# Kernel tuning notes

Measured on AMD Instinct MI355X. Metric: run time of the kernel, lower is better.

The kernel has to match this reference:

```python
import jax, jax.numpy as jnp
import numpy as np

B, K, N, M = 32, 128, 128, 256  # batch, num_classes(==n_dim), n_dim, samples-per-matrix
EPSILON = 0.1
LAMBDA_SOFTMAX = 0.1
LEARNING_RATE = 0.01
BN_EPS = 1e-5


def setup_inputs() -> dict:
    key = jax.random.key(0)
    k1, k2, k3 = jax.random.split(key, 3)
    x = jax.random.normal(k1, (B, N, M), dtype=jnp.float32)
    A = jax.random.normal(k2, (K, N, N), dtype=jnp.float32) * 0.1
    EC_proto = jnp.einsum('kij,klj->kil', A, A)  # per-class PSD prototype covariances (K,N,N)
    EC_count = jax.random.uniform(k3, (K,), dtype=jnp.float32, minval=1.0, maxval=100.0)
    return {"x": x, "EC_proto": EC_proto, "EC_count": EC_count}


def reference(x, EC_proto, EC_count):
    n = x.shape[1]
    dtype = x.dtype
    # BatchNorm1d(num_classes, affine=False, track_running_stats=False): batch stats over (N, L)
    mean = x.mean(axis=(0, 2), keepdims=True)
    var = x.var(axis=(0, 2), keepdims=True)  # biased variance, as torch uses for normalization
    x = (x - mean) / jnp.sqrt(var + BN_EPS)

    eye = jnp.eye(n, dtype=dtype)
    total = EC_count.sum()
    has_counts = total > 1e-6

    # E branch: global expansion operator
    e_alpha = jnp.where(has_counts, n / (EPSILON * EPSILON * total), jnp.zeros((), dtype))
    e = e_alpha * jnp.linalg.inv(e_alpha * EC_proto.sum(0) + eye)  # (N,N)
    e_x_z = jnp.einsum('ij,bjm->bim', e, x)  # (B,N,M)

    # C branch: per-class compression operators
    bool_depth = (EC_count != 0).astype(dtype)  # (K,)
    count_fix = EC_count + (1.0 - bool_depth)
    c_alpha = (n / (count_fix * EPSILON * EPSILON) * bool_depth)[:, None, None]  # (K,1,1)
    c = c_alpha * jnp.linalg.inv(c_alpha * EC_proto + eye[None])  # (K,N,N)
    c_x_z = jnp.einsum('kij,bjm->bkim', c, x)  # (B,K,N,M)

    # Frobenius norm per (b,k), rescaled to sum to 10 over classes
    norm = jnp.sqrt((c_x_z * c_x_z).sum(axis=(2, 3)))  # (B,K)
    norm = 10.0 * norm / norm.sum(axis=1, keepdims=True)

    pi = jax.nn.softmax(-LAMBDA_SOFTMAX * norm, axis=1) * bool_depth  # (B,K)
    gama = jnp.where(has_counts, EC_count / total, jnp.zeros_like(EC_count))  # (K,)

    z_d = e_x_z - jnp.einsum('k,bkim,bk->bim', gama, c_x_z, pi)  # (B,N,M)
    return x + LEARNING_RATE * z_d
```

## Files before the change

### kernel.cpp

```cpp
#include <hip/hip_runtime.h>
#include <math.h>

#define Bb 32
#define Kk 128
#define Nn 128
#define Mm 256
#define EPS2 0.01f
#define LAMBDA_S 0.1f
#define LR 0.01f
#define BN_EPS_C 1e-5f

#define SWZ(c) (((c) & 14) | (((c) & 1) << 4) | (((c) >> 4) & 1))

__device__ __forceinline__ float readlane_f(float v, int lane) {
  return __int_as_float(__builtin_amdgcn_readlane(__float_as_int(v), lane));
}

__global__ void kA_bn_psum(const float* __restrict__ x, const float* __restrict__ P,
                           float* __restrict__ xn, float* __restrict__ Psum) {
  int t = threadIdx.x;
  if (blockIdx.x < 128) {
    int n = blockIdx.x;
    float v[32];
    float s = 0.f, s2 = 0.f;
    #pragma unroll
    for (int b = 0; b < Bb; ++b) {
      v[b] = x[(size_t)b * (Nn * Mm) + n * Mm + t];
      s += v[b];
      s2 += v[b] * v[b];
    }
    #pragma unroll
    for (int o = 32; o > 0; o >>= 1) {
      s += __shfl_down(s, o, 64);
      s2 += __shfl_down(s2, o, 64);
    }
    __shared__ float rs[4], rs2[4];
    if ((t & 63) == 0) { rs[t >> 6] = s; rs2[t >> 6] = s2; }
    __syncthreads();
    float S = rs[0] + rs[1] + rs[2] + rs[3];
    float S2 = rs2[0] + rs2[1] + rs2[2] + rs2[3];
    float mean = S * (1.0f / (Bb * Mm));
    float var = S2 * (1.0f / (Bb * Mm)) - mean * mean;
    float rstd = 1.0f / sqrtf(var + BN_EPS_C);
    #pragma unroll
    for (int b = 0; b < Bb; ++b)
      xn[(size_t)b * (Nn * Mm) + n * Mm + t] = (v[b] - mean) * rstd;
  } else {
    int e = (blockIdx.x - 128) * 256 + t;
    float s = 0.f;
    #pragma unroll 8
    for (int k = 0; k < Kk; ++k) s += P[(size_t)k * 16384 + e];
    Psum[e] = s;
  }
}

__global__ __launch_bounds__(512, 1) void k3S(
    const float* __restrict__ P, const float* __restrict__ Psum,
    const float* __restrict__ cnt, float* __restrict__ C,
    const float* __restrict__ xn, float* __restrict__ S) {
  __shared__ __align__(16) float LB[8448];
  int bx = blockIdx.x;
  int t = threadIdx.x;

  if (bx < 129) {
    float* Mt = LB;
    float* Rb = LB + 2112;
    float* redc = LB + 4160;
    int mat = bx;
    int tx = t & 15;
    int wy = t >> 4;

    float cv = cnt[t & 127];
    float sr = cv;
    #pragma unroll
    for (int o = 32; o > 0; o >>= 1) sr += __shfl_down(sr, o, 64);
    if ((t & 63) == 0) redc[t >> 6] = sr;
    __syncthreads();
    float total = redc[0] + redc[1];
    bool has = total > 1e-6f;
    float av;
    if (mat < 128) {
      float c = cnt[mat];
      float bk = (c != 0.0f) ? 1.0f : 0.0f;
      float cfix = c + (1.0f - bk);
      av = (float)Nn / (cfix * EPS2) * bk;
    } else {
      av = has ? ((float)Nn / (EPS2 * total)) : 0.0f;
    }
    const float* src = (mat < 128) ? (P + (size_t)mat * 16384) : Psum;

    float a[4][8];
    #pragma unroll
    for (int i = 0; i < 4; ++i) {
      int row = wy * 4 + i;
      float4 p0 = *(const float4*)&src[row * 128 + tx * 8];
      float4 p1 = *(const float4*)&src[row * 128 + tx * 8 + 4];
      a[i][0] = av * p0.x; a[i][1] = av * p0.y; a[i][2] = av * p0.z; a[i][3] = av * p0.w;
      a[i][4] = av * p1.x; a[i][5] = av * p1.y; a[i][6] = av * p1.z; a[i][7] = av * p1.w;
      if (tx == (wy >> 1)) a[i][(wy & 1) * 4 + i] += 1.0f;
    }

    for (int kb = 0; kb < 8; ++kb) {
      int k0 = kb * 16;
      if ((wy >> 2) == kb) {
        int d = wy & 3;
        #pragma unroll
        for (int i = 0; i < 4; ++i) {
          *(float4*)&Rb[(d * 4 + i) * 128 + SWZ(2 * tx) * 4] =
              make_float4(a[i][0], a[i][1], a[i][2], a[i][3]);
          *(float4*)&Rb[(d * 4 + i) * 128 + SWZ(2 * tx + 1) * 4] =
              make_float4(a[i][4], a[i][5], a[i][6], a[i][7]);
        }
      }
      if ((tx >> 1) == kb) {
        int dh = tx & 1;
        #pragma unroll
        for (int i = 0; i < 4; ++i)
          #pragma unroll
          for (int j = 0; j < 8; ++j)
            Mt[(dh * 8 + j) * 132 + wy * 4 + i] = a[i][j];
      }
      __syncthreads();

      if (t < 64) {
        int l = t;
        float m[2][16];
        #pragma unroll
        for (int d = 0; d < 2; ++d)
          #pragma unroll
          for (int j = 0; j < 16; ++j)
            m[d][j] = Mt[j * 132 + 2 * l + d];
        #pragma unroll
        for (int q = 0; q < 16; ++q) {
          int lq = (k0 + q) >> 1;
          float pr[16];
          #pragma unroll
          for (int j = 0; j < 16; ++j) pr[j] = readlane_f(m[q & 1][j], lq);
          float piv = pr[q];
          float r0 = __builtin_amdgcn_rcpf(piv);
          float pinv = r0 * (2.0f - piv * r0);
          #pragma unroll
          for (int d = 0; d < 2; ++d) {
            float f = m[d][q];
            bool isp = (2 * l + d == k0 + q);
            float g = isp ? (1.0f - pinv) : f * pinv;
            #pragma unroll
            for (int j = 0; j < 16; ++j) m[d][j] = fmaf(-g, pr[j], m[d][j]);
            m[d][q] = isp ? pinv : -g;
          }
        }
        #pragma unroll
        for (int d = 0; d < 2; ++d)
          #pragma unroll
          for (int j = 0; j < 16; ++j)
            Mt[j * 132 + 2 * l + d] = m[d][j];
      }
      __syncthreads();

      if ((wy >> 2) == kb) {
        #pragma unroll
        for (int i = 0; i < 4; ++i)
          #pragma unroll
          for (int j = 0; j < 8; ++j) a[i][j] = 0.0f;
      }
      #pragma unroll
      for (int q = 0; q < 16; ++q) {
        float4 m0 = *(const float4*)&Mt[q * 132 + wy * 4];
        float4 r0 = *(const float4*)&Rb[q * 128 + SWZ(2 * tx) * 4];
        float4 r1 = *(const float4*)&Rb[q * 128 + SWZ(2 * tx + 1) * 4];
        float mq[4] = {m0.x, m0.y, m0.z, m0.w};
        float rq[8] = {r0.x, r0.y, r0.z, r0.w, r1.x, r1.y, r1.z, r1.w};
        #pragma unroll
        for (int i = 0; i < 4; ++i)
          #pragma unroll
          for (int j = 0; j < 8; ++j)
            a[i][j] = fmaf(mq[i], rq[j], a[i][j]);
      }
      if ((tx >> 1) == kb) {
        int dh = tx & 1;
        #pragma unroll
        for (int j = 0; j < 8; ++j) {
          float4 v0 = *(const float4*)&Mt[(dh * 8 + j) * 132 + wy * 4];
          a[0][j] = v0.x; a[1][j] = v0.y; a[2][j] = v0.z; a[3][j] = v0.w;
        }
      }
      __syncthreads();
    }

    float* dst = C + (size_t)mat * 16384;
    #pragma unroll
    for (int i = 0; i < 4; ++i) {
      int row = wy * 4 + i;
      float4 v0 = make_float4(av * a[i][0], av * a[i][1], av * a[i][2], av * a[i][3]);
      float4 v1 = make_float4(av * a[i][4], av * a[i][5], av * a[i][6], av * a[i][7]);
      *(float4*)&dst[row * 128 + tx * 8] = v0;
      *(float4*)&dst[row * 128 + tx * 8 + 4] = v1;
    }
  } else {
    int bxx = bx - 129;
    int b = bxx >> 1;
    int jbase = (bxx & 1) * 64;
    float* X = LB;
    int tx = t & 15, wy = t >> 4;
    float acc[4][4] = {};
    for (int mc = 0; mc < Mm; mc += 64) {
      __syncthreads();
      #pragma unroll
      for (int c = 0; c < 16; ++c) {
        int e = c * 512 + t;
        int i = e >> 6, mm = e & 63;
        X[i * 65 + mm] = xn[(size_t)b * (Nn * Mm) + i * Mm + mc + mm];
      }
      __syncthreads();
      for (int mm = 0; mm < 64; ++mm) {
        float ai[4], bj[4];
        #pragma unroll
        for (int q = 0; q < 4; ++q) ai[q] = X[(wy * 4 + q) * 65 + mm];
        #pragma unroll
        for (int q = 0; q < 4; ++q) bj[q] = X[(jbase + tx * 4 + q) * 65 + mm];
        #pragma unroll
        for (int qi = 0; qi < 4; ++qi)
          #pragma unroll
          for (int qj = 0; qj < 4; ++qj)
            acc[qi][qj] = fmaf(ai[qi], bj[qj], acc[qi][qj]);
      }
    }
    float* dst = S + (size_t)b * 16384;
    #pragma unroll
    for (int qi = 0; qi < 4; ++qi) {
      float4 v = make_float4(acc[qi][0], acc[qi][1], acc[qi][2], acc[qi][3]);
      *(float4*)&dst[(wy * 4 + qi) * 128 + jbase + tx * 4] = v;
    }
  }
}

__global__ __launch_bounds__(256, 1) void kGN(const float* __restrict__ C,
                                              const float* __restrict__ S,
                                              float* __restrict__ norm2h) {
  __shared__ __align__(16) float LB[128 * 128];
  __shared__ float redb[4][32];
  int k = blockIdx.x >> 1, h = blockIdx.x & 1;
  int t = threadIdx.x;
  const float* src = C + (size_t)k * 16384;
  for (int c = 0; c < 64; ++c) LB[c * 256 + t] = src[c * 256 + t];
  __syncthreads();
  int tx = t & 15, ty = t >> 4;
  int i0 = ty * 8, j0 = h * 64 + tx * 4;
  float acc[8][4] = {};
  for (int l = 0; l < 128; ++l) {
    float ai[8], bj[4];
    *(float4*)&ai[0] = *(const float4*)&LB[l * 128 + i0];
    *(float4*)&ai[4] = *(const float4*)&LB[l * 128 + i0 + 4];
    *(float4*)&bj[0] = *(const float4*)&LB[l * 128 + j0];
    #pragma unroll
    for (int qi = 0; qi < 8; ++qi)
      #pragma unroll
      for (int qj = 0; qj < 4; ++qj)
        acc[qi][qj] = fmaf(ai[qi], bj[qj], acc[qi][qj]);
  }
  __syncthreads();
  #pragma unroll
  for (int qi = 0; qi < 8; ++qi)
    *(float4*)&LB[(i0 + qi) * 64 + tx * 4] =
        make_float4(acc[qi][0], acc[qi][1], acc[qi][2], acc[qi][3]);
  __syncthreads();
  float nacc[32];
  #pragma unroll
  for (int b = 0; b < 32; ++b) nacc[b] = 0.0f;
  #pragma unroll
  for (int q = 0; q < 8; ++q) {
    int el = (q * 256 + t) * 4;
    float4 g = *(const float4*)&LB[el];
    int i = el >> 6, jl = el & 63;
    const float* sb = S + i * 128 + h * 64 + jl;
    #pragma unroll
    for (int b = 0; b < 32; ++b) {
      float4 sv = *(const float4*)&sb[(size_t)b * 16384];
      nacc[b] = fmaf(g.x, sv.x, nacc[b]);
      nacc[b] = fmaf(g.y, sv.y, nacc[b]);
      nacc[b] = fmaf(g.z, sv.z, nacc[b]);
      nacc[b] = fmaf(g.w, sv.w, nacc[b]);
    }
  }
  #pragma unroll
  for (int b = 0; b < 32; ++b) {
    float v = nacc[b];
    #pragma unroll
    for (int o = 32; o > 0; o >>= 1) v += __shfl_down(v, o, 64);
    nacc[b] = v;
  }
  if ((t & 63) == 0) {
    int w = t >> 6;
    #pragma unroll
    for (int b = 0; b < 32; ++b) redb[w][b] = nacc[b];
  }
  __syncthreads();
  if (t < 32)
    norm2h[(size_t)k * 64 + h * 32 + t] =
        redb[0][t] + redb[1][t] + redb[2][t] + redb[3][t];
}

__global__ void k7n(const float* __restrict__ norm2h, const float* __restrict__ cnt,
                    float* __restrict__ wT) {
  int b = blockIdx.x;
  int k = threadIdx.x;
  float n2 = norm2h[(size_t)k * 64 + b] + norm2h[(size_t)k * 64 + 32 + b];
  float norm = sqrtf(fmaxf(n2, 0.0f));
  float cv = cnt[k];
  __shared__ float r1[2], r2[2], r3[2];
  float tt = cv, r = norm;
  #pragma unroll
  for (int o = 32; o > 0; o >>= 1) {
    tt += __shfl_down(tt, o, 64);
    r += __shfl_down(r, o, 64);
  }
  if ((k & 63) == 0) { r1[k >> 6] = tt; r2[k >> 6] = r; }
  __syncthreads();
  float total = r1[0] + r1[1];
  float sumn = r2[0] + r2[1];
  float nr = 10.0f * norm / fmaxf(sumn, 1e-30f);
  float ex = expf(-LAMBDA_S * nr);
  float e2 = ex;
  #pragma unroll
  for (int o = 32; o > 0; o >>= 1) e2 += __shfl_down(e2, o, 64);
  if ((k & 63) == 0) r3[k >> 6] = e2;
  __syncthreads();
  float sume = r3[0] + r3[1];
  float bk = (cv != 0.0f) ? 1.0f : 0.0f;
  float pi = (ex / sume) * bk;
  float gama = (total > 1e-6f) ? (cv / total) : 0.0f;
  wT[k * 32 + b] = gama * pi;
}

__global__ __launch_bounds__(256, 1) void k8_k(const float* __restrict__ C,
                                               const float* __restrict__ E,
                                               const float* __restrict__ wT,
                                               float* __restrict__ F) {
  int e = blockIdx.x * 256 + threadIdx.x;
  int b0 = blockIdx.y * 8;
  float acc[8];
  float ev = E[e];
  #pragma unroll
  for (int b = 0; b < 8; ++b) acc[b] = ev;
  for (int k = 0; k < 128; ++k) {
    float cv = C[(size_t)k * 16384 + e];
    const float* wk = wT + k * 32 + b0;
    #pragma unroll
    for (int b = 0; b < 8; ++b) acc[b] = fmaf(-wk[b], cv, acc[b]);
  }
  #pragma unroll
  for (int b = 0; b < 8; ++b) F[(size_t)(b0 + b) * 16384 + e] = acc[b];
}

__global__ __launch_bounds__(256, 1) void k9_k(const float* __restrict__ F,
                                               const float* __restrict__ xn,
                                               float* __restrict__ out) {
  int bx = blockIdx.x;
  int b = bx >> 3, y = bx & 7;
  int mq = y >> 1, ih = y & 1;
  __shared__ __align__(16) float Ft[64 * 68];
  __shared__ __align__(16) float Xt[64 * 68];
  int t = threadIdx.x;
  int tx = t & 15, ty = t >> 4;
  float acc[4][4] = {};
  for (int jc = 0; jc < 128; jc += 64) {
    __syncthreads();
    #pragma unroll
    for (int q = 0; q < 4; ++q) {
      int e = q * 256 + t;
      int i = e >> 4, j4 = e & 15;
      *(float4*)&Ft[i * 68 + j4 * 4] =
          *(const float4*)&F[(size_t)b * 16384 + (ih * 64 + i) * 128 + jc + j4 * 4];
    }
    #pragma unroll
    for (int q = 0; q < 4; ++q) {
      int e = q * 256 + t;
      int jj = e >> 4, m4 = e & 15;
      *(float4*)&Xt[jj * 68 + m4 * 4] =
          *(const float4*)&xn[(size_t)b * (Nn * Mm) + (jc + jj) * Mm + mq * 64 + m4 * 4];
    }
    __syncthreads();
    for (int j4 = 0; j4 < 16; ++j4) {
      float4 fi[4], xm[4];
      #pragma unroll
      for (int r = 0; r < 4; ++r)
        fi[r] = *(const float4*)&Ft[(ty * 4 + r) * 68 + j4 * 4];
      #pragma unroll
      for (int r = 0; r < 4; ++r)
        xm[r] = *(const float4*)&Xt[(j4 * 4 + r) * 68 + tx * 4];
      #pragma unroll
      for (int qi = 0; qi < 4; ++qi) {
        #pragma unroll
        for (int qm = 0; qm < 4; ++qm) {
          float xv = ((const float*)&xm[0])[qm];
          acc[qi][qm] = fmaf(fi[qi].x, xv, acc[qi][qm]);
          xv = ((const float*)&xm[1])[qm];
          acc[qi][qm] = fmaf(fi[qi].y, xv, acc[qi][qm]);
          xv = ((const float*)&xm[2])[qm];
          acc[qi][qm] = fmaf(fi[qi].z, xv, acc[qi][qm]);
          xv = ((const float*)&xm[3])[qm];
          acc[qi][qm] = fmaf(fi[qi].w, xv, acc[qi][qm]);
        }
      }
    }
  }
  int i0 = ih * 64 + ty * 4, m0 = mq * 64 + tx * 4;
  #pragma unroll
  for (int qi = 0; qi < 4; ++qi) {
    float4 xv = *(const float4*)&xn[(size_t)b * (Nn * Mm) + (i0 + qi) * Mm + m0];
    float4 o;
    o.x = fmaf(LR, acc[qi][0], xv.x);
    o.y = fmaf(LR, acc[qi][1], xv.y);
    o.z = fmaf(LR, acc[qi][2], xv.z);
    o.w = fmaf(LR, acc[qi][3], xv.w);
    *(float4*)&out[(size_t)b * (Nn * Mm) + (i0 + qi) * Mm + m0] = o;
  }
}

extern "C" void kernel_launch(void* const* d_in, const int* in_sizes, int n_in,
                              void* d_out, int out_size, void* d_ws, size_t ws_size,
                              hipStream_t stream) {
  const float* x = (const float*)d_in[0];
  const float* P = (const float*)d_in[1];
  const float* cnt = (const float*)d_in[2];
  float* out = (float*)d_out;

  float* ws = (float*)d_ws;
  float* xn = ws;
  float* C = xn + 1048576;
  float* S = C + 2113536;
  float* norm2h = S + 524288;
  float* wT = norm2h + 8192;
  float* F = wT + 4096;
  float* Psum = F + 524288;
  size_t need_bytes = (size_t)((Psum + 16384) - ws) * sizeof(float);
  if (ws_size < need_bytes) return;

  hipLaunchKernelGGL(kA_bn_psum, dim3(192), dim3(256), 0, stream, x, P, xn, Psum);
  hipLaunchKernelGGL(k3S, dim3(193), dim3(512), 0, stream, P, Psum, cnt, C, xn, S);
  hipLaunchKernelGGL(kGN, dim3(256), dim3(256), 0, stream, C, S, norm2h);
  hipLaunchKernelGGL(k7n, dim3(32), dim3(128), 0, stream, norm2h, cnt, wT);
  hipLaunchKernelGGL(k8_k, dim3(64, 4), dim3(256), 0, stream, C,
                     C + (size_t)128 * 16384, wT, F);
  hipLaunchKernelGGL(k9_k, dim3(256), dim3(256), 0, stream, F, xn, out);
}
```

Before: 160.6 us.

## Fuse softmax-weight kernel into F accumulation and widen Gram-norm kernel

Removes the separate k7n launch by recomputing the per-batch softmax/gamma weights inside each k8f block (for its 8 batches) and storing them in shared memory. kGN now uses 512 threads with a 4x4 register tile and consumes the C^T C tile directly from registers against S, dropping the shared-memory store/reload and two barriers. The cost is that each k8f block redundantly recomputes the weights for its 8 batches, adding reductions and barriers before the main loop.

```diff
diff --git a/kernel.cpp b/kernel.cpp
--- a/kernel.cpp
+++ b/kernel.cpp
@@ -234,52 +234,43 @@
   }
 }
 
-__global__ __launch_bounds__(256, 1) void kGN(const float* __restrict__ C,
+__global__ __launch_bounds__(512, 1) void kGN(const float* __restrict__ C,
                                               const float* __restrict__ S,
                                               float* __restrict__ norm2h) {
   __shared__ __align__(16) float LB[128 * 128];
-  __shared__ float redb[4][32];
+  __shared__ float redb[8][32];
   int k = blockIdx.x >> 1, h = blockIdx.x & 1;
   int t = threadIdx.x;
   const float* src = C + (size_t)k * 16384;
-  for (int c = 0; c < 64; ++c) LB[c * 256 + t] = src[c * 256 + t];
+  #pragma unroll
+  for (int c = 0; c < 32; ++c) LB[c * 512 + t] = src[c * 512 + t];
   __syncthreads();
   int tx = t & 15, ty = t >> 4;
-  int i0 = ty * 8, j0 = h * 64 + tx * 4;
-  float acc[8][4] = {};
+  int i0 = ty * 4, j0 = h * 64 + tx * 4;
+  float acc[4][4] = {};
   for (int l = 0; l < 128; ++l) {
-    float ai[8], bj[4];
+    float ai[4], bj[4];
     *(float4*)&ai[0] = *(const float4*)&LB[l * 128 + i0];
-    *(float4*)&ai[4] = *(const float4*)&LB[l * 128 + i0 + 4];
     *(float4*)&bj[0] = *(const float4*)&LB[l * 128 + j0];
     #pragma unroll
-    for (int qi = 0; qi < 8; ++qi)
+    for (int qi = 0; qi < 4; ++qi)
       #pragma unroll
       for (int qj = 0; qj < 4; ++qj)
         acc[qi][qj] = fmaf(ai[qi], bj[qj], acc[qi][qj]);
   }
-  __syncthreads();
-  #pragma unroll
-  for (int qi = 0; qi < 8; ++qi)
-    *(float4*)&LB[(i0 + qi) * 64 + tx * 4] =
-        make_float4(acc[qi][0], acc[qi][1], acc[qi][2], acc[qi][3]);
-  __syncthreads();
   float nacc[32];
   #pragma unroll
   for (int b = 0; b < 32; ++b) nacc[b] = 0.0f;
   #pragma unroll
-  for (int q = 0; q < 8; ++q) {
-    int el = (q * 256 + t) * 4;
-    float4 g = *(const float4*)&LB[el];
-    int i = el >> 6, jl = el & 63;
-    const float* sb = S + i * 128 + h * 64 + jl;
+  for (int qi = 0; qi < 4; ++qi) {
+    const float* sb = S + (i0 + qi) * 128 + j0;
     #pragma unroll
     for (int b = 0; b < 32; ++b) {
       float4 sv = *(const float4*)&sb[(size_t)b * 16384];
-      nacc[b] = fmaf(g.x, sv.x, nacc[b]);
-      nacc[b] = fmaf(g.y, sv.y, nacc[b]);
-      nacc[b] = fmaf(g.z, sv.z, nacc[b]);
-      nacc[b] = fmaf(g.w, sv.w, nacc[b]);
+      nacc[b] = fmaf(acc[qi][0], sv.x, nacc[b]);
+      nacc[b] = fmaf(acc[qi][1], sv.y, nacc[b]);
+      nacc[b] = fmaf(acc[qi][2], sv.z, nacc[b]);
+      nacc[b] = fmaf(acc[qi][3], sv.w, nacc[b]);
     }
   }
   #pragma unroll
@@ -295,58 +286,98 @@
     for (int b = 0; b < 32; ++b) redb[w][b] = nacc[b];
   }
   __syncthreads();
-  if (t < 32)
-    norm2h[(size_t)k * 64 + h * 32 + t] =
-        redb[0][t] + redb[1][t] + redb[2][t] + redb[3][t];
-}
-
-__global__ void k7n(const float* __restrict__ norm2h, const float* __restrict__ cnt,
-                    float* __restrict__ wT) {
-  int b = blockIdx.x;
-  int k = threadIdx.x;
-  float n2 = norm2h[(size_t)k * 64 + b] + norm2h[(size_t)k * 64 + 32 + b];
-  float norm = sqrtf(fmaxf(n2, 0.0f));
-  float cv = cnt[k];
-  __shared__ float r1[2], r2[2], r3[2];
-  float tt = cv, r = norm;
-  #pragma unroll
-  for (int o = 32; o > 0; o >>= 1) {
-    tt += __shfl_down(tt, o, 64);
-    r += __shfl_down(r, o, 64);
-  }
-  if ((k & 63) == 0) { r1[k >> 6] = tt; r2[k >> 6] = r; }
+  if (t < 32) {
+    float s = 0.f;
+    #pragma unroll
+    for (int w = 0; w < 8; ++w) s += redb[w][t];
+    norm2h[(size_t)k * 64 + h * 32 + t] = s;
+  }
+}
+
+__global__ __launch_bounds__(256, 1) void k8f(const float* __restrict__ C,
+                                              const float* __restrict__ E,
+                                              const float* __restrict__ norm2h,
+                                              const float* __restrict__ cnt,
+                                              float* __restrict__ F) {
+  int t = threadIdx.x;
+  int e = blockIdx.x * 256 + t;
+  int b0 = blockIdx.y * 8;
+  __shared__ float wTl[128][8];
+  __shared__ float redT[2];
+  __shared__ float redN[2][8];
+  __shared__ float redE[2][8];
+
+  float nb[8];
+  float cv = 0.f;
+  if (t < 128) {
+    int k = t;
+    cv = cnt[k];
+    #pragma unroll
+    for (int j = 0; j < 8; ++j) {
+      float n2 = norm2h[(size_t)k * 64 + b0 + j] +
+                 norm2h[(size_t)k * 64 + 32 + b0 + j];
+      nb[j] = sqrtf(fmaxf(n2, 0.0f));
+    }
+    float tt = cv;
+    float sn[8];
+    #pragma unroll
+    for (int j = 0; j < 8; ++j) sn[j] = nb[j];
+    #pragma unroll
+    for (int o = 32; o > 0; o >>= 1) {
+      tt += __shfl_down(tt, o, 64);
+      #pragma unroll
+      for (int j = 0; j < 8; ++j) sn[j] += __shfl_down(sn[j], o, 64);
+    }
+    if ((t & 63) == 0) {
+      redT[t >> 6] = tt;
+      #pragma unroll
+      for (int j = 0; j < 8; ++j) redN[t >> 6][j] = sn[j];
+    }
+  }
   __syncthreads();
-  float total = r1[0] + r1[1];
-  float sumn = r2[0] + r2[1];
-  float nr = 10.0f * norm / fmaxf(sumn, 1e-30f);
-  float ex = expf(-LAMBDA_S * nr);
-  float e2 = ex;
-  #pragma unroll
-  for (int o = 32; o > 0; o >>= 1) e2 += __shfl_down(e2, o, 64);
-  if ((k & 63) == 0) r3[k >> 6] = e2;
+  float exj[8];
+  if (t < 128) {
+    #pragma unroll
+    for (int j = 0; j < 8; ++j) {
+      float sumn = fmaxf(redN[0][j] + redN[1][j], 1e-30f);
+      float nr = 10.0f * nb[j] / sumn;
+      exj[j] = expf(-LAMBDA_S * nr);
+    }
+    float se[8];
+    #pragma unroll
+    for (int j = 0; j < 8; ++j) se[j] = exj[j];
+    #pragma unroll
+    for (int o = 32; o > 0; o >>= 1) {
+      #pragma unroll
+      for (int j = 0; j < 8; ++j) se[j] += __shfl_down(se[j], o, 64);
+    }
+    if ((t & 63) == 0) {
+      #pragma unroll
+      for (int j = 0; j < 8; ++j) redE[t >> 6][j] = se[j];
+    }
+  }
   __syncthreads();
-  float sume = r3[0] + r3[1];
-  float bk = (cv != 0.0f) ? 1.0f : 0.0f;
-  float pi = (ex / sume) * bk;
-  float gama = (total > 1e-6f) ? (cv / total) : 0.0f;
-  wT[k * 32 + b] = gama * pi;
-}
-
-__global__ __launch_bounds__(256, 1) void k8_k(const float* __restrict__ C,
-                                               const float* __restrict__ E,
-                                               const float* __restrict__ wT,
-                                               float* __restrict__ F) {
-  int e = blockIdx.x * 256 + threadIdx.x;
-  int b0 = blockIdx.y * 8;
+  if (t < 128) {
+    float total = redT[0] + redT[1];
+    float bk = (cv != 0.0f) ? 1.0f : 0.0f;
+    float gama = (total > 1e-6f) ? (cv / total) : 0.0f;
+    #pragma unroll
+    for (int j = 0; j < 8; ++j) {
+      float sume = redE[0][j] + redE[1][j];
+      float pi = (exj[j] / sume) * bk;
+      wTl[t][j] = gama * pi;
+    }
+  }
+  __syncthreads();
+
   float acc[8];
   float ev = E[e];
   #pragma unroll
   for (int b = 0; b < 8; ++b) acc[b] = ev;
   for (int k = 0; k < 128; ++k) {
-    float cv = C[(size_t)k * 16384 + e];
-    const float* wk = wT + k * 32 + b0;
-    #pragma unroll
-    for (int b = 0; b < 8; ++b) acc[b] = fmaf(-wk[b], cv, acc[b]);
+    float cval = C[(size_t)k * 16384 + e];
+    #pragma unroll
+    for (int b = 0; b < 8; ++b) acc[b] = fmaf(-wTl[k][b], cval, acc[b]);
   }
   #pragma unroll
   for (int b = 0; b < 8; ++b) F[(size_t)(b0 + b) * 16384 + e] = acc[b];
@@ -430,17 +461,15 @@
   float* C = xn + 1048576;
   float* S = C + 2113536;
   float* norm2h = S + 524288;
-  float* wT = norm2h + 8192;
-  float* F = wT + 4096;
+  float* F = norm2h + 8192;
   float* Psum = F + 524288;
   size_t need_bytes = (size_t)((Psum + 16384) - ws) * sizeof(float);
   if (ws_size < need_bytes) return;
 
   hipLaunchKernelGGL(kA_bn_psum, dim3(192), dim3(256), 0, stream, x, P, xn, Psum);
   hipLaunchKernelGGL(k3S, dim3(193), dim3(512), 0, stream, P, Psum, cnt, C, xn, S);
-  hipLaunchKernelGGL(kGN, dim3(256), dim3(256), 0, stream, C, S, norm2h);
-  hipLaunchKernelGGL(k7n, dim3(32), dim3(128), 0, stream, norm2h, cnt, wT);
-  hipLaunchKernelGGL(k8_k, dim3(64, 4), dim3(256), 0, stream, C,
-                     C + (size_t)128 * 16384, wT, F);
+  hipLaunchKernelGGL(kGN, dim3(256), dim3(512), 0, stream, C, S, norm2h);
+  hipLaunchKernelGGL(k8f, dim3(64, 4), dim3(256), 0, stream, C,
+                     C + (size_t)128 * 16384, norm2h, cnt, F);
   hipLaunchKernelGGL(k9_k, dim3(256), dim3(256), 0, stream, F, xn, out);
 }
```

Result: no change. 163.4 us (+1.7%).
